# Kernel optimization log

Measured on AMD Instinct MI355X. Metric: run time of the kernel, lower is better.

Reference implementation:

```python
import jax, jax.numpy as jnp
import numpy as np

H, KD, VD = 8, 64, 64
W = 1.25  # custom weight scale


def layer_norm(x, g, b, eps=1e-5):
    m = x.mean(-1, keepdims=True)
    v = ((x - m) ** 2).mean(-1, keepdims=True)
    return (x - m) * jax.lax.rsqrt(v + eps) * g + b


def cross_attention(x1, x2, wq, wk, wv, wo, bo, wm):
    # Conv1d kernel_size=1 == matmul; channel axis splits as (heads, dim)
    b, s1, _ = x1.shape
    s2 = x2.shape[1]
    q = (x1 @ wq.T).reshape(b, s1, H, KD).transpose(0, 2, 1, 3)  # bhqk
    k = (x2 @ wk.T).reshape(b, s2, H, KD).transpose(0, 2, 1, 3)
    v = (x2 @ wv.T).reshape(b, s2, H, VD).transpose(0, 2, 1, 3)
    attn = jnp.einsum('bhqd,bhsd->bhqs', q, k) * (1.0 / (KD ** 0.5))
    attn = jax.nn.softmax(attn * wm, axis=-1)  # elementwise weight BEFORE softmax
    o = jnp.einsum('bhqs,bhsv->bhqv', attn, v)
    o = o.transpose(0, 2, 1, 3).reshape(b, s1, H * VD)
    return o @ wo.T + bo


def make_wm1(nvars, sl2, patch_num):
    sl = sl2 // 2
    wm = jnp.ones((nvars, sl2), jnp.float32)
    wm = wm.at[:2 * patch_num, :sl].multiply(W)
    wm = wm.at[2 * patch_num:, sl:].multiply(W)
    return wm[None, None]  # broadcast over batch, heads


def make_wm2(nvars, sv, patch_num, patch_num_v):
    wm = jnp.ones((nvars, sv), jnp.float32)
    wm = wm.at[:patch_num, :patch_num_v].multiply(W)
    wm = wm.at[patch_num:2 * patch_num, patch_num_v:2 * patch_num_v].multiply(W)
    wm = wm.at[2 * patch_num:, 2 * patch_num_v:].multiply(W)
    return wm[None, None]


def forward(cords_features, spatial_features, speed_features,
            wq1, wk1, wv1, wo1, bo1, wq2, wk2, wv2, wo2, bo2,
            ln1_g, ln1_b, ln2_g, ln2_b, ln3_g, ln3_b,
            ffn_w1, ffn_b1, ffn_w2, ffn_b2):
    b, nvars, d = cords_features.shape
    patch_num = nvars // 3
    patch_num_v = speed_features.shape[1] // 3
    wm1 = make_wm1(nvars, spatial_features.shape[1], patch_num)
    wm2 = make_wm2(nvars, 3 * patch_num_v, patch_num, patch_num_v)
    x = cross_attention(cords_features, spatial_features, wq1, wk1, wv1, wo1, bo1, wm1)
    x = layer_norm(x + cords_features, ln1_g, ln1_b)
    r2 = x
    x = cross_attention(x, speed_features, wq2, wk2, wv2, wo2, bo2, wm2)
    x = layer_norm(x + r2, ln2_g, ln2_b)
    r3 = x
    h = jax.nn.gelu(x @ ffn_w1.T + ffn_b1, approximate=False)
    x = h @ ffn_w2.T + ffn_b2
    return layer_norm(x + r3, ln3_g, ln3_b)


def setup_inputs():
    key = jax.random.key(0)
    ks = jax.random.split(key, 16)
    D, DF = 512, 2048
    s = 0.02
    inp = {
        'cords_features': jax.random.normal(ks[0], (8, 768, D), jnp.float32),
        'spatial_features': jax.random.normal(ks[1], (8, 1024, D), jnp.float32),
        'speed_features': jax.random.normal(ks[2], (8, 768, D), jnp.float32),
        'wq1': jax.random.normal(ks[3], (H * KD, D)) * s,
        'wk1': jax.random.normal(ks[4], (H * KD, D)) * s,
        'wv1': jax.random.normal(ks[5], (H * VD, D)) * s,
        'wo1': jax.random.normal(ks[6], (D, H * VD)) * s,
        'bo1': jnp.zeros((D,), jnp.float32),
        'wq2': jax.random.normal(ks[7], (H * KD, D)) * s,
        'wk2': jax.random.normal(ks[8], (H * KD, D)) * s,
        'wv2': jax.random.normal(ks[9], (H * VD, D)) * s,
        'wo2': jax.random.normal(ks[10], (D, H * VD)) * s,
        'bo2': jnp.zeros((D,), jnp.float32),
        'ln1_g': jnp.ones((D,), jnp.float32), 'ln1_b': jnp.zeros((D,), jnp.float32),
        'ln2_g': jnp.ones((D,), jnp.float32), 'ln2_b': jnp.zeros((D,), jnp.float32),
        'ln3_g': jnp.ones((D,), jnp.float32), 'ln3_b': jnp.zeros((D,), jnp.float32),
        'ffn_w1': jax.random.normal(ks[11], (DF, D)) * s,
        'ffn_b1': jnp.zeros((DF,), jnp.float32),
        'ffn_w2': jax.random.normal(ks[12], (D, DF)) * s,
        'ffn_b2': jnp.zeros((D,), jnp.float32),
    }
    return inp


def reference(cords_features, spatial_features, speed_features,
              wq1, wk1, wv1, wo1, bo1, wq2, wk2, wv2, wo2, bo2,
              ln1_g, ln1_b, ln2_g, ln2_b, ln3_g, ln3_b,
              ffn_w1, ffn_b1, ffn_w2, ffn_b2):
    return forward(cords_features, spatial_features, speed_features,
                   wq1, wk1, wv1, wo1, bo1, wq2, wk2, wv2, wo2, bo2,
                   ln1_g, ln1_b, ln2_g, ln2_b, ln3_g, ln3_b,
                   ffn_w1, ffn_b1, ffn_w2, ffn_b2)
```

## Files before the change

### kernel.cpp

```cpp
#include <hip/hip_runtime.h>
#include <hip/hip_bf16.h>


#define LN_EPS 1e-5f
#define WSCALE 1.25f

typedef __attribute__((ext_vector_type(8))) short short8;
typedef __attribute__((ext_vector_type(4))) float floatx4;
typedef unsigned short us;

__device__ __forceinline__ float bf2f(us u) {
    union { unsigned int i; float f; } v; v.i = ((unsigned int)u) << 16; return v.f;
}
__device__ __forceinline__ us f2bf(float f) {
    union { float f; unsigned int i; } v; v.f = f;
    return (us)((v.i + 0x7FFFu + ((v.i >> 16) & 1u)) >> 16);
}

struct CastArgs {
    const float* src[13];
    us* dst[13];
    int blk_ofs[14];
};
__global__ __launch_bounds__(256) void cast_all(CastArgs a)
{
    int b = blockIdx.x;
    int e = 0;
    while (b >= a.blk_ofs[e + 1]) ++e;
    int i = ((b - a.blk_ofs[e]) * 256 + threadIdx.x) * 8;
    const float* s = a.src[e];
    us* d = a.dst[e];
    float4 x = *(const float4*)(s + i);
    float4 y = *(const float4*)(s + i + 4);
    *(ushort4*)(d + i)     = make_ushort4(f2bf(x.x), f2bf(x.y), f2bf(x.z), f2bf(x.w));
    *(ushort4*)(d + i + 4) = make_ushort4(f2bf(y.x), f2bf(y.y), f2bf(y.z), f2bf(y.w));
}

template<int BM, int BN>
__global__ __launch_bounds__(256) void gemm_t(
    const us* __restrict__ A, const us* __restrict__ Bw,
    const float* __restrict__ bias, float* __restrict__ Cf,
    us* __restrict__ Cb, int M, int N, int K, int flags,
    int vS, us* __restrict__ Vtg)
{
    constexpr int WN = BN / 2;
    constexpr int MT = 4;
    constexpr int NT = WN / 16;
    constexpr int CA = BM / 32;
    constexpr int CB = BN / 32;

    __shared__ us As[BM * 64];
    __shared__ us Bs[BN * 64];

    int t = threadIdx.x;
    int wave = t >> 6, lane = t & 63;
    int m0 = blockIdx.y * BM, n0 = blockIdx.x * BN;
    int wr = (wave >> 1) * 64, wc = (wave & 1) * WN;

    int r_in = lane >> 3;
    int pq   = lane & 7;
    const us* gA[CA]; us* lA[CA];
#pragma unroll
    for (int c = 0; c < CA; ++c) {
        int r = 32 * c + 8 * wave + r_in;
        int q = pq ^ (r & 7);
        gA[c] = A + (size_t)(m0 + r) * K + 8 * q;
        lA[c] = As + (32 * c + 8 * wave) * 64;
    }
    const us* gB[CB]; us* lB[CB];
#pragma unroll
    for (int c = 0; c < CB; ++c) {
        int r = 32 * c + 8 * wave + r_in;
        int q = pq ^ (r & 7);
        gB[c] = Bw + (size_t)(n0 + r) * K + 8 * q;
        lB[c] = Bs + (32 * c + 8 * wave) * 64;
    }

    int fcol = lane & 15, fj = lane >> 4;
    int aoff[MT][2], boff[NT][2];
#pragma unroll
    for (int mt = 0; mt < MT; ++mt)
#pragma unroll
        for (int kc = 0; kc < 2; ++kc) {
            int fr = wr + 16 * mt + fcol;
            aoff[mt][kc] = fr * 64 + ((kc * 4 + fj) ^ (fr & 7)) * 8;
        }
#pragma unroll
    for (int nt = 0; nt < NT; ++nt)
#pragma unroll
        for (int kc = 0; kc < 2; ++kc) {
            int br = wc + 16 * nt + fcol;
            boff[nt][kc] = br * 64 + ((kc * 4 + fj) ^ (br & 7)) * 8;
        }

    floatx4 acc[MT][NT] = {};

    for (int k0 = 0; k0 < K; k0 += 64) {
        __syncthreads();
#pragma unroll
        for (int c = 0; c < CA; ++c)
            __builtin_amdgcn_global_load_lds(
                (const __attribute__((address_space(1))) void*)(gA[c] + k0),
                (__attribute__((address_space(3))) void*)lA[c], 16, 0, 0);
#pragma unroll
        for (int c = 0; c < CB; ++c)
            __builtin_amdgcn_global_load_lds(
                (const __attribute__((address_space(1))) void*)(gB[c] + k0),
                (__attribute__((address_space(3))) void*)lB[c], 16, 0, 0);
        __syncthreads();

        short8 af[MT][2], bfr[NT][2];
#pragma unroll
        for (int mt = 0; mt < MT; ++mt)
#pragma unroll
            for (int kc = 0; kc < 2; ++kc)
                af[mt][kc] = *(const short8*)(As + aoff[mt][kc]);
#pragma unroll
        for (int nt = 0; nt < NT; ++nt)
#pragma unroll
            for (int kc = 0; kc < 2; ++kc)
                bfr[nt][kc] = *(const short8*)(Bs + boff[nt][kc]);
#pragma unroll
        for (int kc = 0; kc < 2; ++kc)
#pragma unroll
            for (int mt = 0; mt < MT; ++mt)
#pragma unroll
                for (int nt = 0; nt < NT; ++nt)
                    acc[mt][nt] = __builtin_amdgcn_mfma_f32_16x16x32_bf16(
                        af[mt][kc], bfr[nt][kc], acc[mt][nt], 0, 0, 0);
    }

    int rq = lane >> 4;
    if (flags & 8) {
        int b = m0 / vS;
        int s_base = m0 - b * vS;
        if (n0 < 512) {
#pragma unroll
            for (int mt = 0; mt < MT; ++mt)
#pragma unroll
                for (int nt = 0; nt < NT; ++nt) {
                    int col = n0 + wc + 16 * nt + fcol;
#pragma unroll
                    for (int r = 0; r < 4; ++r) {
                        int rloc = wr + 16 * mt + rq * 4 + r;
                        Cb[(size_t)(m0 + rloc) * 512 + col] = f2bf(acc[mt][nt][r]);
                    }
                }
        } else {
#pragma unroll
            for (int mt = 0; mt < MT; ++mt)
#pragma unroll
                for (int nt = 0; nt < NT; ++nt) {
                    int cv = n0 + wc + 16 * nt + fcol - 512;
                    int hv = cv >> 6, dv = cv & 63;
                    int sb = s_base + wr + 16 * mt + rq * 4;
                    ushort4 pk = make_ushort4(
                        f2bf(acc[mt][nt][0]), f2bf(acc[mt][nt][1]),
                        f2bf(acc[mt][nt][2]), f2bf(acc[mt][nt][3]));
                    *(ushort4*)(Vtg + ((size_t)(b * 8 + hv) * 64 + dv) * vS + sb) = pk;
                }
        }
        return;
    }

#pragma unroll
    for (int mt = 0; mt < MT; ++mt)
#pragma unroll
        for (int nt = 0; nt < NT; ++nt) {
            int col = n0 + wc + 16 * nt + fcol;
            float bv = (flags & 1) ? bias[col] : 0.f;
#pragma unroll
            for (int r = 0; r < 4; ++r) {
                int row = m0 + wr + 16 * mt + rq * 4 + r;
                float v = acc[mt][nt][r] + bv;
                if (flags & 2) v = 0.5f * v * (1.0f + erff(v * 0.70710678118654752f));
                if (flags & 4) Cb[(size_t)row * N + col] = f2bf(v);
                else           Cf[(size_t)row * N + col] = v;
            }
        }
}

__global__ __launch_bounds__(256, 4) void attn_kernel(
    const us* __restrict__ Q, const us* __restrict__ Kf,
    const us* __restrict__ Vg, us* __restrict__ O,
    int S1, int S2, int shift)
{
    __shared__ us Qs[64 * 64];
    __shared__ us Ks[64 * 64];
    __shared__ us Vs[64 * 64];
    __shared__ us Ps[64 * 72];

    int t = threadIdx.x;
    int wave = t >> 6, lane = t & 63;
    int quad = lane >> 4, l15 = lane & 15;
    int q0 = blockIdx.x * 64, hh = blockIdx.y, bb = blockIdx.z;
    int qb = wave * 16;

    int r_in = lane >> 3, pq = lane & 7;
    const us *gK[2], *gV[2];
    us *lK[2], *lV[2];
#pragma unroll
    for (int c2 = 0; c2 < 2; ++c2) {
        int r = qb + 8 * c2 + r_in;
        int lq = pq ^ (r & 7);
        const us* gQ = Q + ((size_t)bb * S1 + q0 + r) * 512 + hh * 64 + 8 * lq;
        gK[c2] = Kf + ((size_t)bb * S2 + r) * 512 + hh * 64 + 8 * lq;
        gV[c2] = Vg + ((size_t)(bb * 8 + hh) * 64 + r) * S2 + 8 * lq;
        us* lQ = Qs + (qb + 8 * c2) * 64;
        lK[c2] = Ks + (qb + 8 * c2) * 64;
        lV[c2] = Vs + (qb + 8 * c2) * 64;
        __builtin_amdgcn_global_load_lds(
            (const __attribute__((address_space(1))) void*)gQ,
            (__attribute__((address_space(3))) void*)lQ, 16, 0, 0);
    }

    int aoffQ[2], poffP[2], boff[4][2];
#pragma unroll
    for (int kc = 0; kc < 2; ++kc) {
        int ph = ((kc * 4 + quad) ^ (l15 & 7)) * 8;
        aoffQ[kc] = (qb + l15) * 64 + ph;
        poffP[kc] = (qb + l15) * 72 + ph;
#pragma unroll
        for (int nt = 0; nt < 4; ++nt)
            boff[nt][kc] = (16 * nt + l15) * 64 + ph;
    }
    int pwoff[4][4];
#pragma unroll
    for (int r = 0; r < 4; ++r) {
        int row = qb + quad * 4 + r;
#pragma unroll
        for (int nt = 0; nt < 4; ++nt) {
            int s = 16 * nt + l15;
            pwoff[nt][r] = row * 72 + (((s >> 3) ^ (row & 7)) * 8) + (s & 7);
        }
    }

    floatx4 acc_o[4] = {};
    float l_part[4] = {0.f, 0.f, 0.f, 0.f};
    int qsh[4];
#pragma unroll
    for (int r = 0; r < 4; ++r) qsh[r] = (q0 + qb + quad * 4 + r) >> shift;

    __syncthreads();
    short8 aq0 = *(const short8*)(Qs + aoffQ[0]);
    short8 aq1 = *(const short8*)(Qs + aoffQ[1]);

    for (int c = 0; c < S2; c += 64) {
        __syncthreads();
#pragma unroll
        for (int c2 = 0; c2 < 2; ++c2) {
            __builtin_amdgcn_global_load_lds(
                (const __attribute__((address_space(1))) void*)(gK[c2] + (size_t)c * 512),
                (__attribute__((address_space(3))) void*)lK[c2], 16, 0, 0);
            __builtin_amdgcn_global_load_lds(
                (const __attribute__((address_space(1))) void*)(gV[c2] + c),
                (__attribute__((address_space(3))) void*)lV[c2], 16, 0, 0);
        }
        __syncthreads();

        floatx4 s_acc[4] = {};
#pragma unroll
        for (int nt = 0; nt < 4; ++nt) {
            short8 bk0 = *(const short8*)(Ks + boff[nt][0]);
            short8 bk1 = *(const short8*)(Ks + boff[nt][1]);
            s_acc[nt] = __builtin_amdgcn_mfma_f32_16x16x32_bf16(aq0, bk0, s_acc[nt], 0, 0, 0);
            s_acc[nt] = __builtin_amdgcn_mfma_f32_16x16x32_bf16(aq1, bk1, s_acc[nt], 0, 0, 0);
        }

#pragma unroll
        for (int nt = 0; nt < 4; ++nt) {
            int srs = (c + 16 * nt + l15) >> shift;
#pragma unroll
            for (int r = 0; r < 4; ++r) {
                float fct = (qsh[r] == srs) ? (0.125f * WSCALE) : 0.125f;
                float p = __expf(s_acc[nt][r] * fct);
                s_acc[nt][r] = p;
                l_part[r] += p;
            }
        }

#pragma unroll
        for (int nt = 0; nt < 4; ++nt)
#pragma unroll
            for (int r = 0; r < 4; ++r)
                Ps[pwoff[nt][r]] = f2bf(s_acc[nt][r]);
        __builtin_amdgcn_wave_barrier();

        short8 ap0 = *(const short8*)(Ps + poffP[0]);
        short8 ap1 = *(const short8*)(Ps + poffP[1]);
#pragma unroll
        for (int nt = 0; nt < 4; ++nt) {
            short8 bv0 = *(const short8*)(Vs + boff[nt][0]);
            short8 bv1 = *(const short8*)(Vs + boff[nt][1]);
            acc_o[nt] = __builtin_amdgcn_mfma_f32_16x16x32_bf16(ap0, bv0, acc_o[nt], 0, 0, 0);
            acc_o[nt] = __builtin_amdgcn_mfma_f32_16x16x32_bf16(ap1, bv1, acc_o[nt], 0, 0, 0);
        }
    }

#pragma unroll
    for (int r = 0; r < 4; ++r) {
#pragma unroll
        for (int off = 8; off; off >>= 1)
            l_part[r] += __shfl_xor(l_part[r], off, 16);
    }
#pragma unroll
    for (int r = 0; r < 4; ++r) {
        float inv = 1.0f / l_part[r];
        size_t base = ((size_t)bb * S1 + q0 + qb + quad * 4 + r) * 512 + hh * 64;
#pragma unroll
        for (int nt = 0; nt < 4; ++nt)
            O[base + 16 * nt + l15] = f2bf(acc_o[nt][r] * inv);
    }
}

__global__ __launch_bounds__(256) void ln_kernel(
    const float* __restrict__ X, const float* __restrict__ R,
    const float* __restrict__ g, const float* __restrict__ bta,
    float* __restrict__ out, us* __restrict__ outb)
{
    int row = blockIdx.x;
    int t   = threadIdx.x;
    const float* xr = X + (size_t)row * 512;
    const float* rr = R + (size_t)row * 512;
    float v0 = xr[t] + rr[t];
    float v1 = xr[t + 256] + rr[t + 256];
    float s  = v0 + v1;
    float sq = v0 * v0 + v1 * v1;
#pragma unroll
    for (int off = 32; off; off >>= 1) {
        s  += __shfl_xor(s, off, 64);
        sq += __shfl_xor(sq, off, 64);
    }
    __shared__ float ps[4], psq[4];
    int w = t >> 6;
    if ((t & 63) == 0) { ps[w] = s; psq[w] = sq; }
    __syncthreads();
    float S  = ps[0] + ps[1] + ps[2] + ps[3];
    float SQ = psq[0] + psq[1] + psq[2] + psq[3];
    float mean = S * (1.0f / 512.0f);
    float var  = SQ * (1.0f / 512.0f) - mean * mean;
    float inv  = rsqrtf(var + LN_EPS);
    float y0 = (v0 - mean) * inv * g[t] + bta[t];
    float y1 = (v1 - mean) * inv * g[t + 256] + bta[t + 256];
    out[(size_t)row * 512 + t]       = y0;
    out[(size_t)row * 512 + t + 256] = y1;
    if (outb) {
        outb[(size_t)row * 512 + t]       = f2bf(y0);
        outb[(size_t)row * 512 + t + 256] = f2bf(y1);
    }
}

extern "C" void kernel_launch(void* const* d_in, const int* in_sizes, int n_in,
                              void* d_out, int out_size, void* d_ws, size_t ws_size,
                              hipStream_t stream)
{
    const float* cords   = (const float*)d_in[0];
    const float* spatial = (const float*)d_in[1];
    const float* speed   = (const float*)d_in[2];
    const float* wq1 = (const float*)d_in[3];
    const float* wk1 = (const float*)d_in[4];
    const float* wv1 = (const float*)d_in[5];
    const float* wo1 = (const float*)d_in[6];
    const float* bo1 = (const float*)d_in[7];
    const float* wq2 = (const float*)d_in[8];
    const float* wk2 = (const float*)d_in[9];
    const float* wv2 = (const float*)d_in[10];
    const float* wo2 = (const float*)d_in[11];
    const float* bo2 = (const float*)d_in[12];
    const float* ln1g = (const float*)d_in[13];
    const float* ln1b = (const float*)d_in[14];
    const float* ln2g = (const float*)d_in[15];
    const float* ln2b = (const float*)d_in[16];
    const float* ln3g = (const float*)d_in[17];
    const float* ln3b = (const float*)d_in[18];
    const float* fw1 = (const float*)d_in[19];
    const float* fb1 = (const float*)d_in[20];
    const float* fw2 = (const float*)d_in[21];
    const float* fb2 = (const float*)d_in[22];

    const int B = 8, S1 = 768, S2 = 1024, Sv = 768, D = 512, DF = 2048;
    const int M1 = B * S1;
    const int M2 = B * S2;

    char* w = (char*)d_ws;
    us* q_bf = (us*)w;              w += (size_t)M1 * D * 2;
    us* k_bf = (us*)w;              w += (size_t)M2 * D * 2;
    us* vt   = (us*)w;              w += (size_t)M2 * D * 2;
    us* o_bf = (us*)w;              w += (size_t)M1 * D * 2;
    float* p  = (float*)w;          w += (size_t)M1 * D * 4;
    float* x1 = (float*)w;          w += (size_t)M1 * D * 4;
    us* cords_bf   = (us*)w;        w += (size_t)M1 * D * 2;
    us* spatial_bf = (us*)w;        w += (size_t)M2 * D * 2;
    us* speed_bf   = (us*)w;        w += (size_t)M1 * D * 2;
    us* wq1b = (us*)w;              w += (size_t)D * D * 2;
    us* wk1b = (us*)w;              w += (size_t)D * D * 2;
    us* wv1b = (us*)w;              w += (size_t)D * D * 2;
    us* wo1b = (us*)w;              w += (size_t)D * D * 2;
    us* wq2b = (us*)w;              w += (size_t)D * D * 2;
    us* wk2b = (us*)w;              w += (size_t)D * D * 2;
    us* wv2b = (us*)w;              w += (size_t)D * D * 2;
    us* wo2b = (us*)w;              w += (size_t)D * D * 2;
    us* fw1b = (us*)w;              w += (size_t)DF * D * 2;
    us* fw2b = (us*)w;              w += (size_t)DF * D * 2;

    us* h_bf  = q_bf;
    float* y  = p;
    us* x1_bf = spatial_bf;
    us* x2_bf = cords_bf;
    float* x2 = (float*)d_out;

    dim3 blk(256);

    {
        CastArgs ca;
        const float* srcs[13] = {cords, spatial, speed, wq1, wk1, wv1, wo1,
                                 wq2, wk2, wv2, wo2, fw1, fw2};
        us* dsts[13] = {cords_bf, spatial_bf, speed_bf, wq1b, wk1b, wv1b, wo1b,
                        wq2b, wk2b, wv2b, wo2b, fw1b, fw2b};
        int ns[13] = {M1 * D, M2 * D, M1 * D, D * D, D * D, D * D, D * D,
                      D * D, D * D, D * D, D * D, DF * D, DF * D};
        int ofs = 0;
        for (int i = 0; i < 13; ++i) {
            ca.src[i] = srcs[i]; ca.dst[i] = dsts[i];
            ca.blk_ofs[i] = ofs; ofs += ns[i] / 2048;
        }
        ca.blk_ofs[13] = ofs;
        cast_all<<<dim3(ofs), blk, 0, stream>>>(ca);
    }

    auto g128 = [](int M, int N) { return dim3(N / 128, M / 128); };
    auto g64  = [](int M, int N) { return dim3(N / 64,  M / 128); };

    gemm_t<128, 64><<<g64(M1, D), blk, 0, stream>>>(cords_bf, wq1b, nullptr, nullptr, q_bf,
                                                    M1, D, D, 4, 0, nullptr);
    gemm_t<128, 128><<<g128(M2, 1024), blk, 0, stream>>>(spatial_bf, wk1b, nullptr, nullptr, k_bf,
                                                         M2, 1024, D, 8, S2, vt);
    attn_kernel<<<dim3(S1 / 64, 8, B), blk, 0, stream>>>(q_bf, k_bf, vt, o_bf, S1, S2, 9);
    gemm_t<128, 64><<<g64(M1, D), blk, 0, stream>>>(o_bf, wo1b, bo1, p, nullptr,
                                                    M1, D, D, 1, 0, nullptr);
    ln_kernel<<<M1, blk, 0, stream>>>(p, cords, ln1g, ln1b, x1, x1_bf);

    gemm_t<128, 64><<<g64(M1, D), blk, 0, stream>>>(x1_bf, wq2b, nullptr, nullptr, q_bf,
                                                    M1, D, D, 4, 0, nullptr);
    gemm_t<128, 128><<<g128(M1, 1024), blk, 0, stream>>>(speed_bf, wk2b, nullptr, nullptr, k_bf,
                                                         M1, 1024, D, 8, Sv, vt);
    attn_kernel<<<dim3(S1 / 64, 8, B), blk, 0, stream>>>(q_bf, k_bf, vt, o_bf, S1, Sv, 8);
    gemm_t<128, 64><<<g64(M1, D), blk, 0, stream>>>(o_bf, wo2b, bo2, p, nullptr,
                                                    M1, D, D, 1, 0, nullptr);
    ln_kernel<<<M1, blk, 0, stream>>>(p, x1, ln2g, ln2b, x2, x2_bf);

    gemm_t<128, 128><<<g128(M1, DF), blk, 0, stream>>>(x2_bf, fw1b, fb1, nullptr, h_bf,
                                                       M1, DF, D, 1 | 2 | 4, 0, nullptr);
    gemm_t<128, 64><<<g64(M1, D), blk, 0, stream>>>(h_bf, fw2b, fb2, y, nullptr,
                                                    M1, D, DF, 1, 0, nullptr);
    ln_kernel<<<M1, blk, 0, stream>>>(y, x2, ln3g, ln3b, (float*)d_out, nullptr);

    (void)in_sizes; (void)n_in; (void)out_size; (void)ws_size;
}
```

Before: 389.6 us.

## Add 64x64 GEMM tile, emit bf16 pre-LN outputs, approximate erf in GELU

Adds a 64x64-tile bf16 MFMA GEMM kernel and uses it for all N=512 projections, doubling the block count so the GPU is better occupied. Those GEMMs now write bf16 instead of fp32 for the pre-layernorm tensors, halving that traffic, and ln_kernel reads bf16 input. The exact erff in the FFN GELU epilogue is replaced with an Abramowitz-Stegun polynomial plus __expf. Risks are reduced precision before the residual and layernorm, and a less-pipelined GEMM with smaller tiles and less reuse.

```diff
diff --git a/kernel.cpp b/kernel.cpp
--- a/kernel.cpp
+++ b/kernel.cpp
@@ -15,6 +15,16 @@
 __device__ __forceinline__ us f2bf(float f) {
     union { float f; unsigned int i; } v; v.f = f;
     return (us)((v.i + 0x7FFFu + ((v.i >> 16) & 1u)) >> 16);
+}
+__device__ __forceinline__ float gelu_f(float v) {
+    float x  = v * 0.70710678118654752f;
+    float ax = fabsf(x);
+    float t  = 1.0f / (1.0f + 0.3275911f * ax);
+    float p  = t * (0.254829592f + t * (-0.284496736f + t * (1.421413741f +
+               t * (-1.453152027f + t * 1.061405429f))));
+    float er = 1.0f - p * __expf(-ax * ax);
+    er = copysignf(er, x);
+    return 0.5f * v * (1.0f + er);
 }
 
 struct CastArgs {
@@ -36,6 +46,93 @@
     *(ushort4*)(d + i + 4) = make_ushort4(f2bf(y.x), f2bf(y.y), f2bf(y.z), f2bf(y.w));
 }
 
+__global__ __launch_bounds__(256) void gemm64(
+    const us* __restrict__ A, const us* __restrict__ Bw,
+    const float* __restrict__ bias, us* __restrict__ Cb,
+    int M, int N, int K, int flags)
+{
+    __shared__ us As[64 * 64];
+    __shared__ us Bs[64 * 64];
+
+    int t = threadIdx.x;
+    int wave = t >> 6, lane = t & 63;
+    int m0 = blockIdx.y * 64, n0 = blockIdx.x * 64;
+    int wr = (wave >> 1) * 32, wc = (wave & 1) * 32;
+
+    int r_in = lane >> 3;
+    int pq   = lane & 7;
+    const us* gA[2]; const us* gB[2];
+    us* lA[2]; us* lB[2];
+#pragma unroll
+    for (int c = 0; c < 2; ++c) {
+        int r = 16 * wave + 8 * c + r_in;
+        int q = pq ^ (r & 7);
+        gA[c] = A  + (size_t)(m0 + r) * K + 8 * q;
+        gB[c] = Bw + (size_t)(n0 + r) * K + 8 * q;
+        lA[c] = As + (16 * wave + 8 * c) * 64;
+        lB[c] = Bs + (16 * wave + 8 * c) * 64;
+    }
+
+    int fcol = lane & 15, fj = lane >> 4;
+    int aoff[2][2], boff[2][2];
+#pragma unroll
+    for (int mt = 0; mt < 2; ++mt)
+#pragma unroll
+        for (int kc = 0; kc < 2; ++kc) {
+            int fr = wr + 16 * mt + fcol;
+            aoff[mt][kc] = fr * 64 + ((kc * 4 + fj) ^ (fr & 7)) * 8;
+            int br = wc + 16 * mt + fcol;
+            boff[mt][kc] = br * 64 + ((kc * 4 + fj) ^ (br & 7)) * 8;
+        }
+
+    floatx4 acc[2][2] = {};
+
+    for (int k0 = 0; k0 < K; k0 += 64) {
+        __syncthreads();
+#pragma unroll
+        for (int c = 0; c < 2; ++c) {
+            __builtin_amdgcn_global_load_lds(
+                (const __attribute__((address_space(1))) void*)(gA[c] + k0),
+                (__attribute__((address_space(3))) void*)lA[c], 16, 0, 0);
+            __builtin_amdgcn_global_load_lds(
+                (const __attribute__((address_space(1))) void*)(gB[c] + k0),
+                (__attribute__((address_space(3))) void*)lB[c], 16, 0, 0);
+        }
+        __syncthreads();
+
+        short8 af[2][2], bfr[2][2];
+#pragma unroll
+        for (int mt = 0; mt < 2; ++mt)
+#pragma unroll
+            for (int kc = 0; kc < 2; ++kc) {
+                af[mt][kc]  = *(const short8*)(As + aoff[mt][kc]);
+                bfr[mt][kc] = *(const short8*)(Bs + boff[mt][kc]);
+            }
+#pragma unroll
+        for (int kc = 0; kc < 2; ++kc)
+#pragma unroll
+            for (int mt = 0; mt < 2; ++mt)
+#pragma unroll
+                for (int nt = 0; nt < 2; ++nt)
+                    acc[mt][nt] = __builtin_amdgcn_mfma_f32_16x16x32_bf16(
+                        af[mt][kc], bfr[nt][kc], acc[mt][nt], 0, 0, 0);
+    }
+
+    int rq = lane >> 4;
+#pragma unroll
+    for (int mt = 0; mt < 2; ++mt)
+#pragma unroll
+        for (int nt = 0; nt < 2; ++nt) {
+            int col = n0 + wc + 16 * nt + fcol;
+            float bv = (flags & 1) ? bias[col] : 0.f;
+#pragma unroll
+            for (int r = 0; r < 4; ++r) {
+                int row = m0 + wr + 16 * mt + rq * 4 + r;
+                Cb[(size_t)row * N + col] = f2bf(acc[mt][nt][r] + bv);
+            }
+        }
+}
+
 template<int BM, int BN>
 __global__ __launch_bounds__(256) void gemm_t(
     const us* __restrict__ A, const us* __restrict__ Bw,
@@ -173,7 +270,7 @@
             for (int r = 0; r < 4; ++r) {
                 int row = m0 + wr + 16 * mt + rq * 4 + r;
                 float v = acc[mt][nt][r] + bv;
-                if (flags & 2) v = 0.5f * v * (1.0f + erff(v * 0.70710678118654752f));
+                if (flags & 2) v = gelu_f(v);
                 if (flags & 4) Cb[(size_t)row * N + col] = f2bf(v);
                 else           Cf[(size_t)row * N + col] = v;
             }
@@ -314,16 +411,16 @@
 }
 
 __global__ __launch_bounds__(256) void ln_kernel(
-    const float* __restrict__ X, const float* __restrict__ R,
+    const us* __restrict__ X, const float* __restrict__ R,
     const float* __restrict__ g, const float* __restrict__ bta,
     float* __restrict__ out, us* __restrict__ outb)
 {
     int row = blockIdx.x;
     int t   = threadIdx.x;
-    const float* xr = X + (size_t)row * 512;
+    const us*    xr = X + (size_t)row * 512;
     const float* rr = R + (size_t)row * 512;
-    float v0 = xr[t] + rr[t];
-    float v1 = xr[t + 256] + rr[t + 256];
+    float v0 = bf2f(xr[t]) + rr[t];
+    float v1 = bf2f(xr[t + 256]) + rr[t + 256];
     float s  = v0 + v1;
     float sq = v0 * v0 + v1 * v1;
 #pragma unroll
@@ -387,7 +484,7 @@
     us* k_bf = (us*)w;              w += (size_t)M2 * D * 2;
     us* vt   = (us*)w;              w += (size_t)M2 * D * 2;
     us* o_bf = (us*)w;              w += (size_t)M1 * D * 2;
-    float* p  = (float*)w;          w += (size_t)M1 * D * 4;
+    us* p_bf = (us*)w;              w += (size_t)M1 * D * 2;
     float* x1 = (float*)w;          w += (size_t)M1 * D * 4;
     us* cords_bf   = (us*)w;        w += (size_t)M1 * D * 2;
     us* spatial_bf = (us*)w;        w += (size_t)M2 * D * 2;
@@ -404,7 +501,7 @@
     us* fw2b = (us*)w;              w += (size_t)DF * D * 2;
 
     us* h_bf  = q_bf;
-    float* y  = p;
+    us* y_bf  = p_bf;
     us* x1_bf = spatial_bf;
     us* x2_bf = cords_bf;
     float* x2 = (float*)d_out;
@@ -428,32 +525,27 @@
         cast_all<<<dim3(ofs), blk, 0, stream>>>(ca);
     }
 
+    auto g64  = [](int M, int N) { return dim3(N / 64,  M / 64); };
     auto g128 = [](int M, int N) { return dim3(N / 128, M / 128); };
-    auto g64  = [](int M, int N) { return dim3(N / 64,  M / 128); };
-
-    gemm_t<128, 64><<<g64(M1, D), blk, 0, stream>>>(cords_bf, wq1b, nullptr, nullptr, q_bf,
-                                                    M1, D, D, 4, 0, nullptr);
+
+    gemm64<<<g64(M1, D), blk, 0, stream>>>(cords_bf, wq1b, nullptr, q_bf, M1, D, D, 0);
     gemm_t<128, 128><<<g128(M2, 1024), blk, 0, stream>>>(spatial_bf, wk1b, nullptr, nullptr, k_bf,
                                                          M2, 1024, D, 8, S2, vt);
     attn_kernel<<<dim3(S1 / 64, 8, B), blk, 0, stream>>>(q_bf, k_bf, vt, o_bf, S1, S2, 9);
-    gemm_t<128, 64><<<g64(M1, D), blk, 0, stream>>>(o_bf, wo1b, bo1, p, nullptr,
-                                                    M1, D, D, 1, 0, nullptr);
-    ln_kernel<<<M1, blk, 0, stream>>>(p, cords, ln1g, ln1b, x1, x1_bf);
-
-    gemm_t<128, 64><<<g64(M1, D), blk, 0, stream>>>(x1_bf, wq2b, nullptr, nullptr, q_bf,
-                                                    M1, D, D, 4, 0, nullptr);
+    gemm64<<<g64(M1, D), blk, 0, stream>>>(o_bf, wo1b, bo1, p_bf, M1, D, D, 1);
+    ln_kernel<<<M1, blk, 0, stream>>>(p_bf, cords, ln1g, ln1b, x1, x1_bf);
+
+    gemm64<<<g64(M1, D), blk, 0, stream>>>(x1_bf, wq2b, nullptr, q_bf, M1, D, D, 0);
     gemm_t<128, 128><<<g128(M1, 1024), blk, 0, stream>>>(speed_bf, wk2b, nullptr, nullptr, k_bf,
                                                          M1, 1024, D, 8, Sv, vt);
     attn_kernel<<<dim3(S1 / 64, 8, B), blk, 0, stream>>>(q_bf, k_bf, vt, o_bf, S1, Sv, 8);
-    gemm_t<128, 64><<<g64(M1, D), blk, 0, stream>>>(o_bf, wo2b, bo2, p, nullptr,
-                                                    M1, D, D, 1, 0, nullptr);
-    ln_kernel<<<M1, blk, 0, stream>>>(p, x1, ln2g, ln2b, x2, x2_bf);
+    gemm64<<<g64(M1, D), blk, 0, stream>>>(o_bf, wo2b, bo2, p_bf, M1, D, D, 1);
+    ln_kernel<<<M1, blk, 0, stream>>>(p_bf, x1, ln2g, ln2b, x2, x2_bf);
 
     gemm_t<128, 128><<<g128(M1, DF), blk, 0, stream>>>(x2_bf, fw1b, fb1, nullptr, h_bf,
                                                        M1, DF, D, 1 | 2 | 4, 0, nullptr);
-    gemm_t<128, 64><<<g64(M1, D), blk, 0, stream>>>(h_bf, fw2b, fb2, y, nullptr,
-                                                    M1, D, DF, 1, 0, nullptr);
-    ln_kernel<<<M1, blk, 0, stream>>>(y, x2, ln3g, ln3b, (float*)d_out, nullptr);
+    gemm64<<<g64(M1, D), blk, 0, stream>>>(h_bf, fw2b, fb2, y_bf, M1, D, DF, 1);
+    ln_kernel<<<M1, blk, 0, stream>>>(y_bf, x2, ln3g, ln3b, (float*)d_out, nullptr);
 
     (void)in_sizes; (void)n_in; (void)out_size; (void)ws_size;
 }
```

New measurement: 367.8 us. 1.06x faster.
